# Kernel optimization log

Measured on AMD Instinct MI355X. Metric: run time of the kernel, lower is better.

The kernel has to match this reference:

```python
import jax, jax.numpy as jnp
import numpy as np

N, E = 10000, 80000
D, D_EDGE, L = 32, 16, 3
D2 = D * D


def layer_norm(x, g, b, eps=1e-5):
    m = jnp.mean(x, axis=-1, keepdims=True)
    v = jnp.var(x, axis=-1, keepdims=True)
    return (x - m) / jnp.sqrt(v + eps) * g + b


def setup_inputs() -> dict:
    key = jax.random.key(0)
    ks = jax.random.split(key, 16)
    s_e = 1.0 / np.sqrt(D_EDGE)
    s_d = 1.0 / np.sqrt(D)
    s_f = 1.0 / np.sqrt(L * D)
    return {
        "x": jax.random.normal(ks[0], (N, D), dtype=jnp.float32),
        "edge_index": jax.random.randint(ks[1], (2, E), 0, N),
        "edge_attr": jax.random.normal(ks[2], (E, D_EDGE), dtype=jnp.float32),
        # shared edge MLP: Linear(d_edge_in -> d^2) + LayerNorm(d^2) + ReLU
        "emlp_w": jax.random.uniform(ks[3], (D2, D_EDGE), jnp.float32, -s_e, s_e),
        "emlp_b": jnp.zeros((D2,), jnp.float32),
        "emlp_ln_g": jnp.ones((D2,), jnp.float32),
        "emlp_ln_b": jnp.zeros((D2,), jnp.float32),
        # per-layer params (stacked over L layers)
        "root_w": jax.random.uniform(ks[4], (L, D, D), jnp.float32, -s_d, s_d),  # NNConv root lin (no bias)
        "conv_b": jnp.zeros((L, D), jnp.float32),                                # NNConv bias
        "res_w": jax.random.uniform(ks[5], (L, D, D), jnp.float32, -s_d, s_d),
        "res_b": jnp.zeros((L, D), jnp.float32),
        "ln_g": jnp.ones((L, D), jnp.float32),
        "ln_b": jnp.zeros((L, D), jnp.float32),
        # fusion: Linear(L*d -> d) + LayerNorm(d) + ReLU
        "fuse_w": jax.random.uniform(ks[6], (D, L * D), jnp.float32, -s_f, s_f),
        "fuse_b": jnp.zeros((D,), jnp.float32),
        "fuse_ln_g": jnp.ones((D,), jnp.float32),
        "fuse_ln_b": jnp.zeros((D,), jnp.float32),
    }


def reference(x, edge_index, edge_attr, emlp_w, emlp_b, emlp_ln_g, emlp_ln_b,
              root_w, conv_b, res_w, res_b, ln_g, ln_b,
              fuse_w, fuse_b, fuse_ln_g, fuse_ln_b):
    n_nodes = x.shape[0]
    src, tgt = edge_index[0], edge_index[1]
    # Shared edge MLP applied to the same edge_attr in every layer -> identical
    # per-edge weight matrices; compute once. [E, d_in, d_out]
    h = layer_norm(edge_attr @ emlp_w.T + emlp_b, emlp_ln_g, emlp_ln_b)
    We = jax.nn.relu(h).reshape(-1, D, D)
    x_src_gatherer = src
    outputs = []
    for l in range(L):
        x_res = x @ res_w[l].T + res_b[l]
        # NNConv message: x_j @ W_e, scatter-add to target nodes
        msg = jnp.einsum('ed,edf->ef', x[x_src_gatherer], We)  # [E, d]
        agg = jax.ops.segment_sum(msg, tgt, num_segments=n_nodes)
        h = agg + x @ root_w[l].T + conv_b[l]
        # dropout is identity in eval mode
        x = layer_norm(h + x_res, ln_g[l], ln_b[l])
        outputs.append(x)
    fused = jnp.concatenate(outputs, axis=-1) @ fuse_w.T + fuse_b
    fused = jax.nn.relu(layer_norm(fused, fuse_ln_g, fuse_ln_b))
    return fused
```

## Files before the change

### kernel.cpp

```cpp
#include <hip/hip_runtime.h>

#define NN 10000
#define EE 80000
#define DD 32
#define DEDGE 16
#define LL 3
#define D2V 1024
#define NTILE 2500

typedef __attribute__((ext_vector_type(8))) short short8v;
typedef __attribute__((ext_vector_type(16))) float f32x16;

__device__ __forceinline__ unsigned short bf16rne(float x) {
    unsigned u = __float_as_uint(x);
    return (unsigned short)((u + 0x7FFF + ((u >> 16) & 1)) >> 16);
}
__device__ __forceinline__ float bf16tof(unsigned short h) {
    return __uint_as_float(((unsigned)h) << 16);
}
__device__ __forceinline__ uint4 pack8(const unsigned short* u) {
    uint4 r;
    r.x = (unsigned)u[0] | ((unsigned)u[1] << 16);
    r.y = (unsigned)u[2] | ((unsigned)u[3] << 16);
    r.z = (unsigned)u[4] | ((unsigned)u[5] << 16);
    r.w = (unsigned)u[6] | ((unsigned)u[7] << 16);
    return r;
}

__global__ __launch_bounds__(1024) void setup_kernel(
    const int* __restrict__ ei,
    const float* __restrict__ emw, const float* __restrict__ emb,
    const float* __restrict__ elg, const float* __restrict__ elb,
    int* __restrict__ cur, int* __restrict__ off, float* __restrict__ st,
    uint4* __restrict__ afh, uint4* __restrict__ afl, uint4* __restrict__ a2f)
{
    __shared__ int smi[NN + 1024];
    const int bid = blockIdx.x;
    const int t = threadIdx.x;

    if (bid == 0) {
        int* cnt = smi;
        int* part = smi + NN;
        for (int i = t; i < NN; i += 1024) cnt[i] = 0;
        __syncthreads();
        for (int e = t; e < EE; e += 1024) atomicAdd(&cnt[ei[EE + e]], 1);
        __syncthreads();
        const int base = t * 10;
        int loc[10];
        int run = 0;
#pragma unroll
        for (int i = 0; i < 10; ++i) {
            const int idx = base + i;
            const int v = (idx < NN) ? cnt[idx] : 0;
            loc[i] = run;
            run += v;
        }
        part[t] = run;
        __syncthreads();
        for (int o = 1; o < 1024; o <<= 1) {
            const int v = (t >= o) ? part[t - o] : 0;
            __syncthreads();
            part[t] += v;
            __syncthreads();
        }
        const int excl = part[t] - run;
#pragma unroll
        for (int i = 0; i < 10; ++i) {
            const int idx = base + i;
            if (idx < NN) {
                off[idx] = excl + loc[i];
                cur[idx] = excl + loc[i];
            }
        }
        if (t == 1023) off[NN] = part[1023];
    } else if (bid == 1) {
        float* ws = (float*)smi;
        float* bs = ((float*)smi) + 2048;
        float accM = 0.f, s = 0.f, q = 0.f, sb = 0.f, sb2 = 0.f;
        for (int c = 0; c < 8; ++c) {
            const int r0 = c * 128;
            for (int i = t; i < 2048; i += 1024) ws[i] = emw[r0 * DEDGE + i];
            if (t < 128) bs[t] = emb[r0 + t];
            __syncthreads();
            if (t < 256) {
                const int k = t >> 4, j = t & 15;
                for (int r = 0; r < 128; ++r)
                    accM = fmaf(ws[r * 16 + k], ws[r * 16 + j], accM);
            } else if (t < 272) {
                const int kk = t - 256;
                for (int r = 0; r < 128; ++r) {
                    s += ws[r * 16 + kk];
                    q = fmaf(bs[r], ws[r * 16 + kk], q);
                }
            } else if (t == 288) {
                for (int r = 0; r < 128; ++r) {
                    sb += bs[r];
                    sb2 = fmaf(bs[r], bs[r], sb2);
                }
            }
            __syncthreads();
        }
        if (t < 256) {
            st[t] = accM * (1.f / D2V);
        } else if (t < 272) {
            st[t] = s * (1.f / D2V);
            st[t + 16] = q * (1.f / D2V);
        } else if (t == 288) {
            st[288] = sb * (1.f / D2V);
            st[289] = sb2 * (1.f / D2V);
        }
    } else {
        const int tid2 = (bid - 2) * 1024 + t;
        const int d = tid2 >> 6, l = tid2 & 63;
        const int row = l & 31, kh = l >> 5;
        const int r = d * 32 + row;
        const float g = elg[r];
        unsigned short uh[8], ul[8];
#pragma unroll
        for (int i = 0; i < 8; ++i) {
            const float v = g * emw[r * DEDGE + kh * 8 + i];
            const unsigned short h = bf16rne(v);
            uh[i] = h;
            ul[i] = bf16rne(v - bf16tof(h));
        }
        afh[d * 64 + l] = pack8(uh);
        afl[d * 64 + l] = pack8(ul);
        if (kh == 0) {
            const float bg = g * emb[r];
            const float lbv = elb[r];
            const unsigned short bgh = bf16rne(bg);
            const unsigned short bgl = bf16rne(bg - bf16tof(bgh));
            const unsigned short gh = bf16rne(g);
            const unsigned short gl = bf16rne(g - bf16tof(gh));
            const unsigned short lbh = bf16rne(lbv);
            const unsigned short lbl = bf16rne(lbv - bf16tof(lbh));
            unsigned short sarr[8] = {bgh, bgl, bgh, gh, gl, gh, lbh, lbl};
            a2f[d * 64 + l] = pack8(sarr);
        } else {
            a2f[d * 64 + l] = make_uint4(0, 0, 0, 0);
        }
    }
}

__global__ __launch_bounds__(256) void stats_edge_perm2(const float* __restrict__ eattr,
                                                        const float* __restrict__ st,
                                                        const int* __restrict__ ei,
                                                        int* __restrict__ cur,
                                                        uint4* __restrict__ bfh,
                                                        uint4* __restrict__ bfl,
                                                        uint4* __restrict__ b2f,
                                                        int* __restrict__ sperm) {
    const int e = blockIdx.x * 256 + threadIdx.x;
    if (e >= EE) return;
    const int tgt = ei[EE + e];
    const int p = atomicAdd(&cur[tgt], 1);
    sperm[p] = ei[e];
    float ea[16];
    {
        const float4* ep = (const float4*)(eattr + e * DEDGE);
#pragma unroll
        for (int c = 0; c < 4; ++c) {
            const float4 t4 = ep[c];
            ea[4 * c] = t4.x; ea[4 * c + 1] = t4.y; ea[4 * c + 2] = t4.z; ea[4 * c + 3] = t4.w;
        }
    }
    float m = st[288];
#pragma unroll
    for (int k = 0; k < 16; ++k) m = fmaf(st[256 + k], ea[k], m);
    float ex2 = st[289];
#pragma unroll
    for (int k = 0; k < 16; ++k) {
        float tv = 2.f * st[272 + k];
#pragma unroll
        for (int j = 0; j < 16; ++j) tv = fmaf(st[k * 16 + j], ea[j], tv);
        ex2 = fmaf(tv, ea[k], ex2);
    }
    const float var = fmaxf(ex2 - m * m, 0.f);
    const float inv = rsqrtf(var + 1e-5f);
    const float nmi = -m * inv;
    const int tt = p >> 5, col = p & 31;
#pragma unroll
    for (int h = 0; h < 2; ++h) {
        unsigned short uh[8], ul[8];
#pragma unroll
        for (int i = 0; i < 8; ++i) {
            const float v = inv * ea[8 * h + i];
            const unsigned short a = bf16rne(v);
            uh[i] = a;
            ul[i] = bf16rne(v - bf16tof(a));
        }
        bfh[tt * 64 + h * 32 + col] = pack8(uh);
        bfl[tt * 64 + h * 32 + col] = pack8(ul);
    }
    const unsigned short ivh = bf16rne(inv);
    const unsigned short ivl = bf16rne(inv - bf16tof(ivh));
    const unsigned short nmh = bf16rne(nmi);
    const unsigned short nml = bf16rne(nmi - bf16tof(nmh));
    const unsigned short one = 0x3F80;
    unsigned short s[8] = {ivh, ivh, ivl, nmh, nmh, nml, one, one};
    b2f[tt * 64 + col] = pack8(s);
    b2f[tt * 64 + 32 + col] = make_uint4(0, 0, 0, 0);
}

__global__ __launch_bounds__(256) void edge_mfma_kernel(
    const float* __restrict__ x, const int* __restrict__ sperm,
    const uint4* __restrict__ afh, const uint4* __restrict__ afl, const uint4* __restrict__ a2f,
    const uint4* __restrict__ bfh, const uint4* __restrict__ bfl, const uint4* __restrict__ b2f,
    float* __restrict__ msgout) {
    const int lane = threadIdx.x & 63;
    const int w = (blockIdx.x * 256 + threadIdx.x) >> 6;
    const int col = lane & 31, hi = lane >> 5;
    const int p = w * 32 + col;
    const int si = sperm[p];
    float xr[32];
    {
        const float4* xp = (const float4*)(x + si * DD);
#pragma unroll
        for (int c = 0; c < 8; ++c) {
            const float4 t4 = xp[c];
            xr[4 * c] = t4.x; xr[4 * c + 1] = t4.y; xr[4 * c + 2] = t4.z; xr[4 * c + 3] = t4.w;
        }
    }
    const short8v bh = ((const short8v*)bfh)[w * 64 + lane];
    const short8v bl = ((const short8v*)bfl)[w * 64 + lane];
    const short8v b2 = ((const short8v*)b2f)[w * 64 + lane];
    float mg[16];
#pragma unroll
    for (int i = 0; i < 16; ++i) mg[i] = 0.f;
#pragma unroll
    for (int d = 0; d < 32; ++d) {
        const short8v ah = ((const short8v*)afh)[d * 64 + lane];
        const short8v al = ((const short8v*)afl)[d * 64 + lane];
        const short8v a2 = ((const short8v*)a2f)[d * 64 + lane];
        f32x16 C;
#pragma unroll
        for (int r = 0; r < 16; ++r) C[r] = 0.f;
        C = __builtin_amdgcn_mfma_f32_32x32x16_bf16(ah, bh, C, 0, 0, 0);
        C = __builtin_amdgcn_mfma_f32_32x32x16_bf16(ah, bl, C, 0, 0, 0);
        C = __builtin_amdgcn_mfma_f32_32x32x16_bf16(al, bh, C, 0, 0, 0);
        C = __builtin_amdgcn_mfma_f32_32x32x16_bf16(a2, b2, C, 0, 0, 0);
        const float xd = xr[d];
#pragma unroll
        for (int r = 0; r < 16; ++r) mg[r] = fmaf(xd, fmaxf(C[r], 0.f), mg[r]);
    }
    float* op = msgout + p * DD + hi * 4;
#pragma unroll
    for (int q = 0; q < 4; ++q)
        *(float4*)(op + q * 8) = make_float4(mg[4 * q], mg[4 * q + 1], mg[4 * q + 2], mg[4 * q + 3]);
}

__global__ __launch_bounds__(256) void node_wave_kernel(
    const float* __restrict__ x, const float* __restrict__ msg,
    const int* __restrict__ off,
    const float* __restrict__ root_w, const float* __restrict__ conv_b,
    const float* __restrict__ res_w, const float* __restrict__ res_b,
    const float* __restrict__ lng, const float* __restrict__ lnb,
    float* __restrict__ out) {
    const int lane = threadIdx.x & 63;
    const int w = (blockIdx.x * 256 + threadIdx.x) >> 6;
    const int hi = lane >> 5, f = lane & 31;
    const int n = w * 2 + hi;
    float wrow[32];
    {
        const float4* rp = (const float4*)(root_w + f * DD);
        const float4* sp = (const float4*)(res_w + f * DD);
#pragma unroll
        for (int c = 0; c < 8; ++c) {
            const float4 a = rp[c];
            const float4 b = sp[c];
            wrow[4 * c] = a.x + b.x; wrow[4 * c + 1] = a.y + b.y;
            wrow[4 * c + 2] = a.z + b.z; wrow[4 * c + 3] = a.w + b.w;
        }
    }
    float acc = conv_b[f] + res_b[f];
    const int k0 = off[n], k1 = off[n + 1];
    for (int k = k0; k < k1; ++k) acc += msg[k * DD + f];
    const float xl = x[n * DD + f];
#pragma unroll
    for (int d = 0; d < DD; ++d) acc = fmaf(__shfl(xl, hi * 32 + d), wrow[d], acc);
    float s1 = acc, s2 = acc * acc;
#pragma unroll
    for (int o = 16; o >= 1; o >>= 1) {
        s1 += __shfl_xor(s1, o);
        s2 += __shfl_xor(s2, o);
    }
    const float m = s1 * (1.f / 32.f);
    const float v = s2 * (1.f / 32.f) - m * m;
    const float inv = rsqrtf(v + 1e-5f);
    out[n * DD + f] = fmaf((acc - m) * inv, lng[f], lnb[f]);
}

__global__ __launch_bounds__(256) void node_fuse_kernel(
    const float* __restrict__ x, const float* __restrict__ msg,
    const int* __restrict__ off,
    const float* __restrict__ root_w, const float* __restrict__ conv_b,
    const float* __restrict__ res_w, const float* __restrict__ res_b,
    const float* __restrict__ lng, const float* __restrict__ lnb,
    const float* __restrict__ o0, const float* __restrict__ o1,
    const float* __restrict__ fw, const float* __restrict__ fb,
    const float* __restrict__ fg, const float* __restrict__ fbb,
    float* __restrict__ out) {
    const int lane = threadIdx.x & 63;
    const int w = (blockIdx.x * 256 + threadIdx.x) >> 6;
    const int hi = lane >> 5, f = lane & 31;
    const int n = w * 2 + hi;
    float o2v;
    {
        float wrow[32];
        {
            const float4* rp = (const float4*)(root_w + f * DD);
            const float4* sp = (const float4*)(res_w + f * DD);
#pragma unroll
            for (int c = 0; c < 8; ++c) {
                const float4 a = rp[c];
                const float4 b = sp[c];
                wrow[4 * c] = a.x + b.x; wrow[4 * c + 1] = a.y + b.y;
                wrow[4 * c + 2] = a.z + b.z; wrow[4 * c + 3] = a.w + b.w;
            }
        }
        float acc = conv_b[f] + res_b[f];
        const int k0 = off[n], k1 = off[n + 1];
        for (int k = k0; k < k1; ++k) acc += msg[k * DD + f];
        const float xl = x[n * DD + f];
#pragma unroll
        for (int d = 0; d < DD; ++d) acc = fmaf(__shfl(xl, hi * 32 + d), wrow[d], acc);
        float s1 = acc, s2 = acc * acc;
#pragma unroll
        for (int o = 16; o >= 1; o >>= 1) {
            s1 += __shfl_xor(s1, o);
            s2 += __shfl_xor(s2, o);
        }
        const float m = s1 * (1.f / 32.f);
        const float v = s2 * (1.f / 32.f) - m * m;
        const float inv = rsqrtf(v + 1e-5f);
        o2v = fmaf((acc - m) * inv, lng[f], lnb[f]);
    }
    float fr[96];
    {
        const float4* fp = (const float4*)(fw + f * 96);
#pragma unroll
        for (int c = 0; c < 24; ++c) {
            const float4 t4 = fp[c];
            fr[4 * c] = t4.x; fr[4 * c + 1] = t4.y; fr[4 * c + 2] = t4.z; fr[4 * c + 3] = t4.w;
        }
    }
    float acc = fb[f];
    const float c0 = o0[n * DD + f], c1 = o1[n * DD + f];
#pragma unroll
    for (int d = 0; d < DD; ++d) acc = fmaf(__shfl(c0, hi * 32 + d), fr[d], acc);
#pragma unroll
    for (int d = 0; d < DD; ++d) acc = fmaf(__shfl(c1, hi * 32 + d), fr[32 + d], acc);
#pragma unroll
    for (int d = 0; d < DD; ++d) acc = fmaf(__shfl(o2v, hi * 32 + d), fr[64 + d], acc);
    float s1 = acc, s2 = acc * acc;
#pragma unroll
    for (int o = 16; o >= 1; o >>= 1) {
        s1 += __shfl_xor(s1, o);
        s2 += __shfl_xor(s2, o);
    }
    const float m = s1 * (1.f / 32.f);
    const float v = s2 * (1.f / 32.f) - m * m;
    const float inv = rsqrtf(v + 1e-5f);
    out[n * DD + f] = fmaxf(fmaf((acc - m) * inv, fg[f], fbb[f]), 0.f);
}

extern "C" void kernel_launch(void* const* d_in, const int* in_sizes, int n_in,
                              void* d_out, int out_size, void* d_ws, size_t ws_size,
                              hipStream_t stream) {
    const float* x   = (const float*)d_in[0];
    const int*   ei  = (const int*)d_in[1];
    const float* ea  = (const float*)d_in[2];
    const float* emw = (const float*)d_in[3];
    const float* emb = (const float*)d_in[4];
    const float* elg = (const float*)d_in[5];
    const float* elb = (const float*)d_in[6];
    const float* rootw = (const float*)d_in[7];
    const float* convb = (const float*)d_in[8];
    const float* resw  = (const float*)d_in[9];
    const float* resb  = (const float*)d_in[10];
    const float* lng   = (const float*)d_in[11];
    const float* lnb   = (const float*)d_in[12];
    const float* fw    = (const float*)d_in[13];
    const float* fb    = (const float*)d_in[14];
    const float* flg   = (const float*)d_in[15];
    const float* flb   = (const float*)d_in[16];
    float* doutp = (float*)d_out;

    const size_t U4N = 2048 * 3 + (size_t)NTILE * 64 * 3;
    const size_t FR0 = U4N * 4;
    const size_t FTOT = FR0 + (size_t)EE * DD + 2 * (size_t)NN * DD + 320;
    const size_t ITOT = 2 * (NN + 1) + 2 * (size_t)EE;
    const size_t PRIMARY_NEED = FTOT * 4 + ITOT * 4 + 256;

    if (ws_size < PRIMARY_NEED) return;

    uint4* u4 = (uint4*)d_ws;
    uint4* afh = u4;
    uint4* afl = afh + 2048;
    uint4* a2f = afl + 2048;
    uint4* bfh = a2f + 2048;
    uint4* bfl = bfh + (size_t)NTILE * 64;
    uint4* b2f = bfl + (size_t)NTILE * 64;
    float* wsf = (float*)d_ws;
    float* msg  = wsf + FR0;
    float* out0 = msg + (size_t)EE * DD;
    float* out1 = out0 + NN * DD;
    float* st   = out1 + NN * DD;
    int* cur   = (int*)(st + 320);
    int* off   = cur + (NN + 1);
    int* spare = off + (NN + 1);
    int* sperm = spare + EE;
    (void)spare;

    setup_kernel<<<4, 1024, 0, stream>>>(ei, emw, emb, elg, elb, cur, off, st,
                                         afh, afl, a2f);
    stats_edge_perm2<<<313, 256, 0, stream>>>(ea, st, ei, cur, bfh, bfl, b2f, sperm);

    edge_mfma_kernel<<<625, 256, 0, stream>>>(x, sperm, afh, afl, a2f, bfh, bfl, b2f, msg);
    node_wave_kernel<<<1250, 256, 0, stream>>>(x, msg, off,
        rootw, convb, resw, resb, lng, lnb, out0);
    edge_mfma_kernel<<<625, 256, 0, stream>>>(out0, sperm, afh, afl, a2f, bfh, bfl, b2f, msg);
    node_wave_kernel<<<1250, 256, 0, stream>>>(out0, msg, off,
        rootw + D2V, convb + DD, resw + D2V, resb + DD, lng + DD, lnb + DD, out1);
    edge_mfma_kernel<<<625, 256, 0, stream>>>(out1, sperm, afh, afl, a2f, bfh, bfl, b2f, msg);
    node_fuse_kernel<<<1250, 256, 0, stream>>>(out1, msg, off,
        rootw + 2 * D2V, convb + 2 * DD, resw + 2 * D2V, resb + 2 * DD,
        lng + 2 * DD, lnb + 2 * DD,
        out0, out1, fw, fb, flg, flb, doutp);
}
```

Before: 174.8 us.

## Parallelize setup across many blocks and batch more work per wave in edge/node kernels

The single-block histogram and weight-statistics setup is split into a many-block kernel using global atomics plus a separate one-block scan, with a memset to zero the counters and stats. The edge MFMA kernel now processes two 32-edge tiles per wave so each A-fragment load is reused twice. The node kernels handle four node pairs per wave, amortizing the weight-row loads. The costs are more register pressure, fewer waves in flight, and two extra launches for the memset and scan.

```diff
diff --git a/kernel.cpp b/kernel.cpp
--- a/kernel.cpp
+++ b/kernel.cpp
@@ -27,98 +27,55 @@
     return r;
 }
 
-__global__ __launch_bounds__(1024) void setup_kernel(
+__global__ __launch_bounds__(256) void setup1_kernel(
     const int* __restrict__ ei,
-    const float* __restrict__ emw, const float* __restrict__ emb,
-    const float* __restrict__ elg, const float* __restrict__ elb,
-    int* __restrict__ cur, int* __restrict__ off, float* __restrict__ st,
-    uint4* __restrict__ afh, uint4* __restrict__ afl, uint4* __restrict__ a2f)
-{
-    __shared__ int smi[NN + 1024];
+    const float* __restrict__ w, const float* __restrict__ wb,
+    const float* __restrict__ lg, const float* __restrict__ lb,
+    int* __restrict__ cnt, float* __restrict__ st,
+    uint4* __restrict__ afh, uint4* __restrict__ afl, uint4* __restrict__ a2f) {
     const int bid = blockIdx.x;
     const int t = threadIdx.x;
-
-    if (bid == 0) {
-        int* cnt = smi;
-        int* part = smi + NN;
-        for (int i = t; i < NN; i += 1024) cnt[i] = 0;
-        __syncthreads();
-        for (int e = t; e < EE; e += 1024) atomicAdd(&cnt[ei[EE + e]], 1);
-        __syncthreads();
-        const int base = t * 10;
-        int loc[10];
-        int run = 0;
-#pragma unroll
-        for (int i = 0; i < 10; ++i) {
-            const int idx = base + i;
-            const int v = (idx < NN) ? cnt[idx] : 0;
-            loc[i] = run;
-            run += v;
-        }
-        part[t] = run;
-        __syncthreads();
-        for (int o = 1; o < 1024; o <<= 1) {
-            const int v = (t >= o) ? part[t - o] : 0;
-            __syncthreads();
-            part[t] += v;
-            __syncthreads();
-        }
-        const int excl = part[t] - run;
-#pragma unroll
-        for (int i = 0; i < 10; ++i) {
-            const int idx = base + i;
-            if (idx < NN) {
-                off[idx] = excl + loc[i];
-                cur[idx] = excl + loc[i];
+    if (bid < 313) {
+        const int e = bid * 256 + t;
+        if (e < EE) atomicAdd(&cnt[ei[EE + e]], 1);
+    } else if (bid < 377) {
+        const int r0 = (bid - 313) * 16;
+        const int k = t >> 4, j = t & 15;
+        float acc = 0.f;
+#pragma unroll
+        for (int r = 0; r < 16; ++r)
+            acc = fmaf(w[(r0 + r) * DEDGE + k], w[(r0 + r) * DEDGE + j], acc);
+        atomicAdd(&st[t], acc * (1.f / D2V));
+        if (t < DEDGE) {
+            float s = 0.f, q = 0.f;
+#pragma unroll
+            for (int r = 0; r < 16; ++r) {
+                s += w[(r0 + r) * DEDGE + t];
+                q = fmaf(wb[r0 + r], w[(r0 + r) * DEDGE + t], q);
             }
-        }
-        if (t == 1023) off[NN] = part[1023];
-    } else if (bid == 1) {
-        float* ws = (float*)smi;
-        float* bs = ((float*)smi) + 2048;
-        float accM = 0.f, s = 0.f, q = 0.f, sb = 0.f, sb2 = 0.f;
-        for (int c = 0; c < 8; ++c) {
-            const int r0 = c * 128;
-            for (int i = t; i < 2048; i += 1024) ws[i] = emw[r0 * DEDGE + i];
-            if (t < 128) bs[t] = emb[r0 + t];
-            __syncthreads();
-            if (t < 256) {
-                const int k = t >> 4, j = t & 15;
-                for (int r = 0; r < 128; ++r)
-                    accM = fmaf(ws[r * 16 + k], ws[r * 16 + j], accM);
-            } else if (t < 272) {
-                const int kk = t - 256;
-                for (int r = 0; r < 128; ++r) {
-                    s += ws[r * 16 + kk];
-                    q = fmaf(bs[r], ws[r * 16 + kk], q);
-                }
-            } else if (t == 288) {
-                for (int r = 0; r < 128; ++r) {
-                    sb += bs[r];
-                    sb2 = fmaf(bs[r], bs[r], sb2);
-                }
+            atomicAdd(&st[256 + t], s * (1.f / D2V));
+            atomicAdd(&st[272 + t], q * (1.f / D2V));
+        } else if (t == 16) {
+            float s = 0.f, s2 = 0.f;
+#pragma unroll
+            for (int r = 0; r < 16; ++r) {
+                s += wb[r0 + r];
+                s2 = fmaf(wb[r0 + r], wb[r0 + r], s2);
             }
-            __syncthreads();
-        }
-        if (t < 256) {
-            st[t] = accM * (1.f / D2V);
-        } else if (t < 272) {
-            st[t] = s * (1.f / D2V);
-            st[t + 16] = q * (1.f / D2V);
-        } else if (t == 288) {
-            st[288] = sb * (1.f / D2V);
-            st[289] = sb2 * (1.f / D2V);
+            atomicAdd(&st[288], s * (1.f / D2V));
+            atomicAdd(&st[289], s2 * (1.f / D2V));
         }
     } else {
-        const int tid2 = (bid - 2) * 1024 + t;
-        const int d = tid2 >> 6, l = tid2 & 63;
+        const int tid = (bid - 377) * 256 + t;
+        if (tid >= 32 * 64) return;
+        const int d = tid >> 6, l = tid & 63;
         const int row = l & 31, kh = l >> 5;
         const int r = d * 32 + row;
-        const float g = elg[r];
+        const float g = lg[r];
         unsigned short uh[8], ul[8];
 #pragma unroll
         for (int i = 0; i < 8; ++i) {
-            const float v = g * emw[r * DEDGE + kh * 8 + i];
+            const float v = g * w[r * DEDGE + kh * 8 + i];
             const unsigned short h = bf16rne(v);
             uh[i] = h;
             ul[i] = bf16rne(v - bf16tof(h));
@@ -126,8 +83,8 @@
         afh[d * 64 + l] = pack8(uh);
         afl[d * 64 + l] = pack8(ul);
         if (kh == 0) {
-            const float bg = g * emb[r];
-            const float lbv = elb[r];
+            const float bg = g * wb[r];
+            const float lbv = lb[r];
             const unsigned short bgh = bf16rne(bg);
             const unsigned short bgl = bf16rne(bg - bf16tof(bgh));
             const unsigned short gh = bf16rne(g);
@@ -140,6 +97,39 @@
             a2f[d * 64 + l] = make_uint4(0, 0, 0, 0);
         }
     }
+}
+
+__global__ __launch_bounds__(1024) void scan_kernel(int* __restrict__ cur, int* __restrict__ off) {
+    __shared__ int s[1024];
+    const int t = threadIdx.x;
+    const int base = t * 10;
+    int loc[10];
+    int run = 0;
+#pragma unroll
+    for (int i = 0; i < 10; ++i) {
+        const int idx = base + i;
+        const int v = (idx < NN) ? cur[idx] : 0;
+        loc[i] = run;
+        run += v;
+    }
+    s[t] = run;
+    __syncthreads();
+    for (int o = 1; o < 1024; o <<= 1) {
+        const int v = (t >= o) ? s[t - o] : 0;
+        __syncthreads();
+        s[t] += v;
+        __syncthreads();
+    }
+    const int excl = s[t] - run;
+#pragma unroll
+    for (int i = 0; i < 10; ++i) {
+        const int idx = base + i;
+        if (idx < NN) {
+            off[idx] = excl + loc[i];
+            cur[idx] = excl + loc[i];
+        }
+    }
+    if (t == 1023) off[NN] = s[1023];
 }
 
 __global__ __launch_bounds__(256) void stats_edge_perm2(const float* __restrict__ eattr,
@@ -202,54 +192,79 @@
     b2f[tt * 64 + 32 + col] = make_uint4(0, 0, 0, 0);
 }
 
-__global__ __launch_bounds__(256) void edge_mfma_kernel(
+__global__ __launch_bounds__(256) void edge_mfma2_kernel(
     const float* __restrict__ x, const int* __restrict__ sperm,
     const uint4* __restrict__ afh, const uint4* __restrict__ afl, const uint4* __restrict__ a2f,
     const uint4* __restrict__ bfh, const uint4* __restrict__ bfl, const uint4* __restrict__ b2f,
     float* __restrict__ msgout) {
     const int lane = threadIdx.x & 63;
-    const int w = (blockIdx.x * 256 + threadIdx.x) >> 6;
+    const int wv = (blockIdx.x * 256 + threadIdx.x) >> 6;
+    if (wv >= NTILE / 2) return;
     const int col = lane & 31, hi = lane >> 5;
-    const int p = w * 32 + col;
-    const int si = sperm[p];
-    float xr[32];
+    const int t0 = wv * 2, t1 = t0 + 1;
+    const int p0 = t0 * 32 + col, p1 = t1 * 32 + col;
+    const int s0 = sperm[p0], s1 = sperm[p1];
+    float xr0[32], xr1[32];
     {
-        const float4* xp = (const float4*)(x + si * DD);
+        const float4* xp0 = (const float4*)(x + s0 * DD);
+        const float4* xp1 = (const float4*)(x + s1 * DD);
 #pragma unroll
         for (int c = 0; c < 8; ++c) {
-            const float4 t4 = xp[c];
-            xr[4 * c] = t4.x; xr[4 * c + 1] = t4.y; xr[4 * c + 2] = t4.z; xr[4 * c + 3] = t4.w;
-        }
-    }
-    const short8v bh = ((const short8v*)bfh)[w * 64 + lane];
-    const short8v bl = ((const short8v*)bfl)[w * 64 + lane];
-    const short8v b2 = ((const short8v*)b2f)[w * 64 + lane];
-    float mg[16];
-#pragma unroll
-    for (int i = 0; i < 16; ++i) mg[i] = 0.f;
+            const float4 a4 = xp0[c];
+            xr0[4 * c] = a4.x; xr0[4 * c + 1] = a4.y; xr0[4 * c + 2] = a4.z; xr0[4 * c + 3] = a4.w;
+            const float4 b4 = xp1[c];
+            xr1[4 * c] = b4.x; xr1[4 * c + 1] = b4.y; xr1[4 * c + 2] = b4.z; xr1[4 * c + 3] = b4.w;
+        }
+    }
+    const short8v bh0 = ((const short8v*)bfh)[t0 * 64 + lane];
+    const short8v bl0 = ((const short8v*)bfl)[t0 * 64 + lane];
+    const short8v b20 = ((const short8v*)b2f)[t0 * 64 + lane];
+    const short8v bh1 = ((const short8v*)bfh)[t1 * 64 + lane];
+    const short8v bl1 = ((const short8v*)bfl)[t1 * 64 + lane];
+    const short8v b21 = ((const short8v*)b2f)[t1 * 64 + lane];
+    float mg0[16], mg1[16];
+#pragma unroll
+    for (int i = 0; i < 16; ++i) { mg0[i] = 0.f; mg1[i] = 0.f; }
 #pragma unroll
     for (int d = 0; d < 32; ++d) {
         const short8v ah = ((const short8v*)afh)[d * 64 + lane];
         const short8v al = ((const short8v*)afl)[d * 64 + lane];
         const short8v a2 = ((const short8v*)a2f)[d * 64 + lane];
-        f32x16 C;
-#pragma unroll
-        for (int r = 0; r < 16; ++r) C[r] = 0.f;
-        C = __builtin_amdgcn_mfma_f32_32x32x16_bf16(ah, bh, C, 0, 0, 0);
-        C = __builtin_amdgcn_mfma_f32_32x32x16_bf16(ah, bl, C, 0, 0, 0);
-        C = __builtin_amdgcn_mfma_f32_32x32x16_bf16(al, bh, C, 0, 0, 0);
-        C = __builtin_amdgcn_mfma_f32_32x32x16_bf16(a2, b2, C, 0, 0, 0);
-        const float xd = xr[d];
-#pragma unroll
-        for (int r = 0; r < 16; ++r) mg[r] = fmaf(xd, fmaxf(C[r], 0.f), mg[r]);
-    }
-    float* op = msgout + p * DD + hi * 4;
-#pragma unroll
-    for (int q = 0; q < 4; ++q)
-        *(float4*)(op + q * 8) = make_float4(mg[4 * q], mg[4 * q + 1], mg[4 * q + 2], mg[4 * q + 3]);
-}
-
-__global__ __launch_bounds__(256) void node_wave_kernel(
+        {
+            f32x16 C;
+#pragma unroll
+            for (int r = 0; r < 16; ++r) C[r] = 0.f;
+            C = __builtin_amdgcn_mfma_f32_32x32x16_bf16(ah, bh0, C, 0, 0, 0);
+            C = __builtin_amdgcn_mfma_f32_32x32x16_bf16(ah, bl0, C, 0, 0, 0);
+            C = __builtin_amdgcn_mfma_f32_32x32x16_bf16(al, bh0, C, 0, 0, 0);
+            C = __builtin_amdgcn_mfma_f32_32x32x16_bf16(a2, b20, C, 0, 0, 0);
+            const float xd = xr0[d];
+#pragma unroll
+            for (int r = 0; r < 16; ++r) mg0[r] = fmaf(xd, fmaxf(C[r], 0.f), mg0[r]);
+        }
+        {
+            f32x16 C;
+#pragma unroll
+            for (int r = 0; r < 16; ++r) C[r] = 0.f;
+            C = __builtin_amdgcn_mfma_f32_32x32x16_bf16(ah, bh1, C, 0, 0, 0);
+            C = __builtin_amdgcn_mfma_f32_32x32x16_bf16(ah, bl1, C, 0, 0, 0);
+            C = __builtin_amdgcn_mfma_f32_32x32x16_bf16(al, bh1, C, 0, 0, 0);
+            C = __builtin_amdgcn_mfma_f32_32x32x16_bf16(a2, b21, C, 0, 0, 0);
+            const float xd = xr1[d];
+#pragma unroll
+            for (int r = 0; r < 16; ++r) mg1[r] = fmaf(xd, fmaxf(C[r], 0.f), mg1[r]);
+        }
+    }
+    float* op0 = msgout + p0 * DD + hi * 4;
+    float* op1 = msgout + p1 * DD + hi * 4;
+#pragma unroll
+    for (int q = 0; q < 4; ++q) {
+        *(float4*)(op0 + q * 8) = make_float4(mg0[4 * q], mg0[4 * q + 1], mg0[4 * q + 2], mg0[4 * q + 3]);
+        *(float4*)(op1 + q * 8) = make_float4(mg1[4 * q], mg1[4 * q + 1], mg1[4 * q + 2], mg1[4 * q + 3]);
+    }
+}
+
+__global__ __launch_bounds__(256) void node_wave4_kernel(
     const float* __restrict__ x, const float* __restrict__ msg,
     const int* __restrict__ off,
     const float* __restrict__ root_w, const float* __restrict__ conv_b,
@@ -257,9 +272,9 @@
     const float* __restrict__ lng, const float* __restrict__ lnb,
     float* __restrict__ out) {
     const int lane = threadIdx.x & 63;
-    const int w = (blockIdx.x * 256 + threadIdx.x) >> 6;
+    const int wv = (blockIdx.x * 256 + threadIdx.x) >> 6;
+    if (wv >= 1250) return;
     const int hi = lane >> 5, f = lane & 31;
-    const int n = w * 2 + hi;
     float wrow[32];
     {
         const float4* rp = (const float4*)(root_w + f * DD);
@@ -272,25 +287,31 @@
             wrow[4 * c + 2] = a.z + b.z; wrow[4 * c + 3] = a.w + b.w;
         }
     }
-    float acc = conv_b[f] + res_b[f];
-    const int k0 = off[n], k1 = off[n + 1];
-    for (int k = k0; k < k1; ++k) acc += msg[k * DD + f];
-    const float xl = x[n * DD + f];
-#pragma unroll
-    for (int d = 0; d < DD; ++d) acc = fmaf(__shfl(xl, hi * 32 + d), wrow[d], acc);
-    float s1 = acc, s2 = acc * acc;
-#pragma unroll
-    for (int o = 16; o >= 1; o >>= 1) {
-        s1 += __shfl_xor(s1, o);
-        s2 += __shfl_xor(s2, o);
-    }
-    const float m = s1 * (1.f / 32.f);
-    const float v = s2 * (1.f / 32.f) - m * m;
-    const float inv = rsqrtf(v + 1e-5f);
-    out[n * DD + f] = fmaf((acc - m) * inv, lng[f], lnb[f]);
-}
-
-__global__ __launch_bounds__(256) void node_fuse_kernel(
+    const float bias = conv_b[f] + res_b[f];
+    const float g = lng[f], bb = lnb[f];
+#pragma unroll
+    for (int i = 0; i < 4; ++i) {
+        const int n = (wv * 4 + i) * 2 + hi;
+        float acc = bias;
+        const int k0 = off[n], k1 = off[n + 1];
+        for (int k = k0; k < k1; ++k) acc += msg[k * DD + f];
+        const float xl = x[n * DD + f];
+#pragma unroll
+        for (int d = 0; d < DD; ++d) acc = fmaf(__shfl(xl, hi * 32 + d), wrow[d], acc);
+        float s1 = acc, s2 = acc * acc;
+#pragma unroll
+        for (int o = 16; o >= 1; o >>= 1) {
+            s1 += __shfl_xor(s1, o);
+            s2 += __shfl_xor(s2, o);
+        }
+        const float m = s1 * (1.f / 32.f);
+        const float v = s2 * (1.f / 32.f) - m * m;
+        const float inv = rsqrtf(v + 1e-5f);
+        out[n * DD + f] = fmaf((acc - m) * inv, g, bb);
+    }
+}
+
+__global__ __launch_bounds__(256) void node_fuse4_kernel(
     const float* __restrict__ x, const float* __restrict__ msg,
     const int* __restrict__ off,
     const float* __restrict__ root_w, const float* __restrict__ conv_b,
@@ -301,29 +322,63 @@
     const float* __restrict__ fg, const float* __restrict__ fbb,
     float* __restrict__ out) {
     const int lane = threadIdx.x & 63;
-    const int w = (blockIdx.x * 256 + threadIdx.x) >> 6;
+    const int wv = (blockIdx.x * 256 + threadIdx.x) >> 6;
+    if (wv >= 1250) return;
     const int hi = lane >> 5, f = lane & 31;
-    const int n = w * 2 + hi;
-    float o2v;
+    float wrow[32];
     {
-        float wrow[32];
+        const float4* rp = (const float4*)(root_w + f * DD);
+        const float4* sp = (const float4*)(res_w + f * DD);
+#pragma unroll
+        for (int c = 0; c < 8; ++c) {
+            const float4 a = rp[c];
+            const float4 b = sp[c];
+            wrow[4 * c] = a.x + b.x; wrow[4 * c + 1] = a.y + b.y;
+            wrow[4 * c + 2] = a.z + b.z; wrow[4 * c + 3] = a.w + b.w;
+        }
+    }
+    float fr[96];
+    {
+        const float4* fp = (const float4*)(fw + f * 96);
+#pragma unroll
+        for (int c = 0; c < 24; ++c) {
+            const float4 t4 = fp[c];
+            fr[4 * c] = t4.x; fr[4 * c + 1] = t4.y; fr[4 * c + 2] = t4.z; fr[4 * c + 3] = t4.w;
+        }
+    }
+    const float bias = conv_b[f] + res_b[f];
+    const float g = lng[f], bb = lnb[f];
+    const float fbv = fb[f], fgv = fg[f], fbbv = fbb[f];
+#pragma unroll
+    for (int i = 0; i < 4; ++i) {
+        const int n = (wv * 4 + i) * 2 + hi;
+        float o2v;
         {
-            const float4* rp = (const float4*)(root_w + f * DD);
-            const float4* sp = (const float4*)(res_w + f * DD);
-#pragma unroll
-            for (int c = 0; c < 8; ++c) {
-                const float4 a = rp[c];
-                const float4 b = sp[c];
-                wrow[4 * c] = a.x + b.x; wrow[4 * c + 1] = a.y + b.y;
-                wrow[4 * c + 2] = a.z + b.z; wrow[4 * c + 3] = a.w + b.w;
+            float acc = bias;
+            const int k0 = off[n], k1 = off[n + 1];
+            for (int k = k0; k < k1; ++k) acc += msg[k * DD + f];
+            const float xl = x[n * DD + f];
+#pragma unroll
+            for (int d = 0; d < DD; ++d) acc = fmaf(__shfl(xl, hi * 32 + d), wrow[d], acc);
+            float s1 = acc, s2 = acc * acc;
+#pragma unroll
+            for (int o = 16; o >= 1; o >>= 1) {
+                s1 += __shfl_xor(s1, o);
+                s2 += __shfl_xor(s2, o);
             }
-        }
-        float acc = conv_b[f] + res_b[f];
-        const int k0 = off[n], k1 = off[n + 1];
-        for (int k = k0; k < k1; ++k) acc += msg[k * DD + f];
-        const float xl = x[n * DD + f];
-#pragma unroll
-        for (int d = 0; d < DD; ++d) acc = fmaf(__shfl(xl, hi * 32 + d), wrow[d], acc);
+            const float m = s1 * (1.f / 32.f);
+            const float v = s2 * (1.f / 32.f) - m * m;
+            const float inv = rsqrtf(v + 1e-5f);
+            o2v = fmaf((acc - m) * inv, g, bb);
+        }
+        float acc = fbv;
+        const float c0 = o0[n * DD + f], c1 = o1[n * DD + f];
+#pragma unroll
+        for (int d = 0; d < DD; ++d) acc = fmaf(__shfl(c0, hi * 32 + d), fr[d], acc);
+#pragma unroll
+        for (int d = 0; d < DD; ++d) acc = fmaf(__shfl(c1, hi * 32 + d), fr[32 + d], acc);
+#pragma unroll
+        for (int d = 0; d < DD; ++d) acc = fmaf(__shfl(o2v, hi * 32 + d), fr[64 + d], acc);
         float s1 = acc, s2 = acc * acc;
 #pragma unroll
         for (int o = 16; o >= 1; o >>= 1) {
@@ -333,35 +388,8 @@
         const float m = s1 * (1.f / 32.f);
         const float v = s2 * (1.f / 32.f) - m * m;
         const float inv = rsqrtf(v + 1e-5f);
-        o2v = fmaf((acc - m) * inv, lng[f], lnb[f]);
-    }
-    float fr[96];
-    {
-        const float4* fp = (const float4*)(fw + f * 96);
-#pragma unroll
-        for (int c = 0; c < 24; ++c) {
-            const float4 t4 = fp[c];
-            fr[4 * c] = t4.x; fr[4 * c + 1] = t4.y; fr[4 * c + 2] = t4.z; fr[4 * c + 3] = t4.w;
-        }
-    }
-    float acc = fb[f];
-    const float c0 = o0[n * DD + f], c1 = o1[n * DD + f];
-#pragma unroll
-    for (int d = 0; d < DD; ++d) acc = fmaf(__shfl(c0, hi * 32 + d), fr[d], acc);
-#pragma unroll
-    for (int d = 0; d < DD; ++d) acc = fmaf(__shfl(c1, hi * 32 + d), fr[32 + d], acc);
-#pragma unroll
-    for (int d = 0; d < DD; ++d) acc = fmaf(__shfl(o2v, hi * 32 + d), fr[64 + d], acc);
-    float s1 = acc, s2 = acc * acc;
-#pragma unroll
-    for (int o = 16; o >= 1; o >>= 1) {
-        s1 += __shfl_xor(s1, o);
-        s2 += __shfl_xor(s2, o);
-    }
-    const float m = s1 * (1.f / 32.f);
-    const float v = s2 * (1.f / 32.f) - m * m;
-    const float inv = rsqrtf(v + 1e-5f);
-    out[n * DD + f] = fmaxf(fmaf((acc - m) * inv, fg[f], fbb[f]), 0.f);
+        out[n * DD + f] = fmaxf(fmaf((acc - m) * inv, fgv, fbbv), 0.f);
+    }
 }
 
 extern "C" void kernel_launch(void* const* d_in, const int* in_sizes, int n_in,
@@ -412,18 +440,19 @@
     int* sperm = spare + EE;
     (void)spare;
 
-    setup_kernel<<<4, 1024, 0, stream>>>(ei, emw, emb, elg, elb, cur, off, st,
-                                         afh, afl, a2f);
+    hipMemsetAsync(st, 0, (320 + NN + 1) * sizeof(float), stream);
+    setup1_kernel<<<385, 256, 0, stream>>>(ei, emw, emb, elg, elb, cur, st, afh, afl, a2f);
+    scan_kernel<<<1, 1024, 0, stream>>>(cur, off);
     stats_edge_perm2<<<313, 256, 0, stream>>>(ea, st, ei, cur, bfh, bfl, b2f, sperm);
 
-    edge_mfma_kernel<<<625, 256, 0, stream>>>(x, sperm, afh, afl, a2f, bfh, bfl, b2f, msg);
-    node_wave_kernel<<<1250, 256, 0, stream>>>(x, msg, off,
+    edge_mfma2_kernel<<<313, 256, 0, stream>>>(x, sperm, afh, afl, a2f, bfh, bfl, b2f, msg);
+    node_wave4_kernel<<<313, 256, 0, stream>>>(x, msg, off,
         rootw, convb, resw, resb, lng, lnb, out0);
-    edge_mfma_kernel<<<625, 256, 0, stream>>>(out0, sperm, afh, afl, a2f, bfh, bfl, b2f, msg);
-    node_wave_kernel<<<1250, 256, 0, stream>>>(out0, msg, off,
+    edge_mfma2_kernel<<<313, 256, 0, stream>>>(out0, sperm, afh, afl, a2f, bfh, bfl, b2f, msg);
+    node_wave4_kernel<<<313, 256, 0, stream>>>(out0, msg, off,
         rootw + D2V, convb + DD, resw + D2V, resb + DD, lng + DD, lnb + DD, out1);
-    edge_mfma_kernel<<<625, 256, 0, stream>>>(out1, sperm, afh, afl, a2f, bfh, bfl, b2f, msg);
-    node_fuse_kernel<<<1250, 256, 0, stream>>>(out1, msg, off,
+    edge_mfma2_kernel<<<313, 256, 0, stream>>>(out1, sperm, afh, afl, a2f, bfh, bfl, b2f, msg);
+    node_fuse4_kernel<<<313, 256, 0, stream>>>(out1, msg, off,
         rootw + 2 * D2V, convb + 2 * DD, resw + 2 * D2V, resb + 2 * DD,
         lng + 2 * DD, lnb + 2 * DD,
         out0, out1, fw, fb, flg, flb, doutp);
```

Measured after the change: 197.9 us. 1.13x slower.
